# Optimization experiments

Hardware: AMD Instinct MI355X
Metric: run time of the kernel (lower is better)

## Reference

```python
import jax, jax.numpy as jnp
import numpy as np

B = 32; N = 512; SEQ_LEN = 8
L = 0.05; T_REF = 5.0; V_TH = 20.0; V_RES = 0.0
SQL = float(np.sqrt(L))
BN_EPS = 1e-5

# ---- Dawson-style lookup tables for the LIF moment activation (built once, float64) ----
_XG = np.linspace(-10.0, 4.0, 7001)
_DX = _XG[1] - _XG[0]

def _cumtrapz(y):
    return np.concatenate([[0.0], np.cumsum(0.5 * (y[1:] + y[:-1]) * _DX)])

_phi = np.exp(-_XG ** 2)
_I = np.exp(-100.0) / 20.0 + _cumtrapz(_phi)          # int_{-inf}^x e^{-t^2} dt (asymptotic tail at -10)
_g = np.exp(_XG ** 2) * _I                             # 1st Dawson-like function g(x)
_G = _cumtrapz(_g)                                     # int g dx (rel. to -10)
_h = np.exp(_XG ** 2) * _cumtrapz(_phi * _g ** 2)      # 2nd Dawson-like function h(x)
_H = _cumtrapz(_h)                                     # int h dx

XG = jnp.asarray(_XG, jnp.float32)
GT = jnp.asarray(_g, jnp.float32)
GI = jnp.asarray(_G, jnp.float32)
HI = jnp.asarray(_H, jnp.float32)

def _interp(x, tab):
    return jnp.interp(x, XG, tab)

def moment_activate(u, s, rho):
    # Mnn_Activate_Mean / Std / Corr: LIF moment activation
    s = jnp.maximum(s, 1e-6)
    ub = jnp.clip((V_TH * L - u) / (s * SQL), -10.0, 4.0)
    lb = jnp.clip((V_RES * L - u) / (s * SQL), -10.0, 4.0)
    dG = _interp(ub, GI) - _interp(lb, GI)
    ua = 1.0 / (T_REF + (2.0 / L) * dG)                               # mean firing rate
    dH = jnp.maximum(_interp(ub, HI) - _interp(lb, HI), 0.0)
    sa = jnp.sqrt((8.0 / L ** 2) * dH * ua ** 3)                      # firing std
    dg = _interp(ub, GT) - _interp(lb, GT)
    chi = ua ** 2 * (2.0 / L) * dg / (SQL * jnp.maximum(sa, 1e-9))    # linear response coeff
    eye = jnp.eye(rho.shape[-1], dtype=rho.dtype)
    rho_out = chi[:, :, None] * chi[:, None, :] * rho                 # [B,N,N]
    rho_out = rho_out * (1.0 - eye) + eye                             # unit diagonal
    return ua, sa, rho_out

def linear_corr(W, b, u, s, rho):
    # Mnn_Linear_Corr: mean via affine map, covariance via W C W^T
    u_out = u @ W.T + b
    Cin = rho * s[:, :, None] * s[:, None, :]                         # [B,N,N] covariance
    C = jnp.einsum('bik,lk->bil', jnp.einsum('ij,bjk->bik', W, Cin), W)
    var = jnp.clip(jnp.diagonal(C, axis1=1, axis2=2), 0.0, None)
    s_out = jnp.sqrt(var)
    denom = s_out[:, :, None] * s_out[:, None, :]
    rho_out = jnp.where(denom > 1e-12, C / jnp.maximum(denom, 1e-12), 0.0)
    return u_out, s_out, rho_out

def mexi_hat(n, k=0.3):
    dx = 2.0 * np.pi / n
    x = np.arange(0.0, 2.0 * np.pi, dx)[:n]
    y = np.exp(2.0 * (np.cos(x) - 1.0)) * np.cos(2.0 * x)
    j = np.arange(n)
    idx = (j[None, :] - j[:, None]) % n                               # w[i,:] = y.roll(i)
    return y[idx].astype(np.float32)

def setup_inputs() -> dict:
    ks = jax.random.split(jax.random.key(0), 10)
    u = jax.random.normal(ks[0], (B, N), jnp.float32)
    s = jax.random.uniform(ks[1], (B, N), jnp.float32, 0.1, 1.0)
    A = jax.random.normal(ks[2], (B, N, N), jnp.float32) / np.sqrt(N)
    sym = 0.5 * (A + jnp.swapaxes(A, 1, 2))
    eye = jnp.eye(N, dtype=jnp.float32)
    rho = jnp.clip(sym, -0.5, 0.5) * (1.0 - eye) + eye                # valid-ish corr matrix
    u_ext = jax.random.normal(ks[3], (B, N), jnp.float32)
    s_ext = jax.random.uniform(ks[4], (B, N), jnp.float32, 0.1, 1.0)
    W = 0.02 * jax.random.normal(ks[5], (N, N), jnp.float32) + 0.1 * jnp.asarray(mexi_hat(N))
    b = 0.02 * jax.random.normal(ks[6], (N,), jnp.float32)
    W_ext = 0.02 * jax.random.normal(ks[7], (N, N), jnp.float32)
    b_ext = 0.02 * jax.random.normal(ks[8], (N,), jnp.float32)
    w_mean = 2.5 * jnp.ones((N,), jnp.float32)
    b_mean = 2.5 * jnp.ones((N,), jnp.float32)
    w_mean_ext = 2.5 * jnp.ones((N,), jnp.float32)
    b_mean_ext = 2.5 * jnp.ones((N,), jnp.float32)
    return {'u': u, 's': s, 'rho': rho, 'u_ext': u_ext, 's_ext': s_ext,
            'W': W, 'b': b, 'W_ext': W_ext, 'b_ext': b_ext,
            'w_mean': w_mean, 'b_mean': b_mean,
            'w_mean_ext': w_mean_ext, 'b_mean_ext': b_mean_ext,
            'seq_len': SEQ_LEN}

def reference(u, s, rho, u_ext, s_ext, W, b, W_ext, b_ext,
              w_mean, b_mean, w_mean_ext, b_mean_ext, seq_len):
    # external pathway (Mnn_Linear_without_Corr + BN), computed once
    u_e = u_ext @ W_ext.T + b_ext
    s_e = jnp.sqrt((s_ext ** 2) @ (W_ext ** 2).T)
    mean_e = jnp.mean(u_e, axis=0); var_e = jnp.var(u_e, axis=0)
    f_e = w_mean_ext / jnp.sqrt(var_e + BN_EPS)
    s_e = s_e * jnp.abs(f_e)                                          # Mnn_Std_Bn1d (uses pre-BN stats)
    u_e = (u_e - mean_e) * f_e + b_mean_ext

    def step(carry, _):
        u, s, rho = carry
        u, s, rho = linear_corr(W, b, u, s, rho)
        mean = jnp.mean(u, axis=0); var = jnp.var(u, axis=0)
        f = w_mean / jnp.sqrt(var + BN_EPS)
        s = s * jnp.abs(f)
        u = (u - mean) * f + b_mean
        u = u + u_e
        s = jnp.sqrt(s * s + s_e * s_e)
        return moment_activate(u, s, rho), None

    (u, s, rho), _ = jax.lax.scan(step, (u, s, rho), None, length=seq_len)
    return u, s, rho
```

## Files before the change

### kernel.cpp

```cpp
#include <hip/hip_runtime.h>
#include <math.h>


#define BB 32
#define NN 512
#define SEQ 8
#define TG 7001
#define SVN (BB * NN)

typedef float f32x4 __attribute__((ext_vector_type(4)));
typedef short s16x8 __attribute__((ext_vector_type(8)));

__device__ __forceinline__ unsigned short bf16_rne(float v) {
    unsigned u = __float_as_uint(v);
    u += 0x7FFFu + ((u >> 16) & 1u);
    return (unsigned short)(u >> 16);
}
__device__ __forceinline__ float bf16_f(unsigned short h) {
    return __uint_as_float(((unsigned)h) << 16);
}
__device__ __forceinline__ void split2(float v, unsigned short& h, unsigned short& l) {
    unsigned short hh = bf16_rne(v);
    h = hh;
    l = bf16_rne(v - bf16_f(hh));
}

__device__ __forceinline__ size_t ts_idx(int r, int k) {
    return (size_t)(((r >> 4) * 16 + (k >> 5)) * 512 + ((k >> 3) & 3) * 128 + (r & 15) * 8 + (k & 7));
}

__device__ __forceinline__ float interp_tab(const float* __restrict__ tab, float x) {
    float t = (x + 10.0f) * 500.0f;
    t = fminf(fmaxf(t, 0.0f), 7000.0f);
    int i0 = (int)t;
    if (i0 > 6999) i0 = 6999;
    float fr = t - (float)i0;
    float a = tab[i0];
    float b = tab[i0 + 1];
    return fmaf(fr, b - a, a);
}

__global__ void k_exp(double* __restrict__ expP, double* __restrict__ expM) {
    int k = blockIdx.x * 256 + threadIdx.x;
    if (k >= TG) return;
    double x = -10.0 + (14.0 / 7000.0) * k;
    expP[k] = exp(x * x);
    expM[k] = exp(-x * x);
}

__device__ double blk_exscan(double part, double* wsum) {
    int t = threadIdx.x, lane = t & 63, wid = t >> 6;
    double run = part;
    #pragma unroll
    for (int off = 1; off < 64; off <<= 1) {
        double nv = __shfl_up(run, off);
        if (lane >= off) run += nv;
    }
    if (lane == 63) wsum[wid] = run;
    __syncthreads();
    if (t < 16) {
        double v = wsum[t];
        #pragma unroll
        for (int off = 1; off < 16; off <<= 1) {
            double nv = __shfl_up(v, off);
            if (lane >= off) v += nv;
        }
        wsum[t] = v;
    }
    __syncthreads();
    double base = (wid > 0) ? wsum[wid - 1] : 0.0;
    double ex = base + run - part;
    __syncthreads();
    return ex;
}

__global__ __launch_bounds__(1024)
void k_scan(const double* __restrict__ expP, const double* __restrict__ expM,
            float* __restrict__ GT, float* __restrict__ GI, float* __restrict__ HI) {
    __shared__ double ys[7008];
    __shared__ double wsum[16];
    const int t = threadIdx.x;
    const double dx = 14.0 / 7000.0;
    int k0 = t * 7, k1 = k0 + 7;
    if (k1 > TG) k1 = TG;
    if (k0 > TG) k0 = TG;
    int kls = (k0 < 1) ? 1 : k0;

    for (int k = k0; k < k1; ++k) ys[k] = expM[k];
    __syncthreads();

    double tmp[7];
    {
        double part = 0.0;
        for (int k = kls; k < k1; ++k) part += 0.5 * (ys[k - 1] + ys[k]) * dx;
        double run = blk_exscan(part, wsum) + exp(-100.0) / 20.0;
        int c = 0;
        for (int k = k0; k < k1; ++k) {
            if (k >= 1) run += 0.5 * (ys[k - 1] + ys[k]) * dx;
            tmp[c] = expP[k] * run;
            GT[k] = (float)tmp[c];
            ++c;
        }
        __syncthreads();
        c = 0;
        for (int k = k0; k < k1; ++k) ys[k] = tmp[c++];
        __syncthreads();
    }
    {
        double part = 0.0;
        for (int k = kls; k < k1; ++k) part += 0.5 * (ys[k - 1] + ys[k]) * dx;
        double run = blk_exscan(part, wsum);
        for (int k = k0; k < k1; ++k) {
            if (k >= 1) run += 0.5 * (ys[k - 1] + ys[k]) * dx;
            GI[k] = (float)run;
        }
        __syncthreads();
    }
    {
        double part = 0.0;
        for (int k = kls; k < k1; ++k) {
            double ya = expM[k - 1] * ys[k - 1] * ys[k - 1];
            double yb = expM[k] * ys[k] * ys[k];
            part += 0.5 * (ya + yb) * dx;
        }
        double run = blk_exscan(part, wsum);
        int c = 0;
        for (int k = k0; k < k1; ++k) {
            if (k >= 1) {
                double ya = expM[k - 1] * ys[k - 1] * ys[k - 1];
                double yb = expM[k] * ys[k] * ys[k];
                run += 0.5 * (ya + yb) * dx;
            }
            tmp[c++] = run;
        }
        __syncthreads();
        c = 0;
        for (int k = k0; k < k1; ++k) ys[k] = tmp[c++];
        __syncthreads();
    }
    {
        double part = 0.0;
        for (int k = kls; k < k1; ++k)
            part += 0.5 * (expP[k - 1] * ys[k - 1] + expP[k] * ys[k]) * dx;
        double run = blk_exscan(part, wsum);
        for (int k = k0; k < k1; ++k) {
            if (k >= 1) run += 0.5 * (expP[k - 1] * ys[k - 1] + expP[k] * ys[k]) * dx;
            HI[k] = (float)run;
        }
    }
}

__global__ void k_splitW(const float* __restrict__ W,
                         unsigned short* __restrict__ Wh, unsigned short* __restrict__ Wl) {
    int t = blockIdx.x * 256 + threadIdx.x;
    int r = t >> 6, c8 = t & 63;
    int k = c8 * 8;
    const float* src = W + (size_t)r * NN + k;
    s16x8 hv, lv;
    #pragma unroll
    for (int q = 0; q < 8; ++q) {
        unsigned short h, l;
        split2(src[q], h, l);
        hv[q] = (short)h; lv[q] = (short)l;
    }
    size_t o = ts_idx(r, k);
    *reinterpret_cast<s16x8*>(Wh + o) = hv;
    *reinterpret_cast<s16x8*>(Wl + o) = lv;
}

__global__ void k_splitQ(const float* __restrict__ rho, const float* __restrict__ s,
                         unsigned short* __restrict__ Qh, unsigned short* __restrict__ Ql) {
    int t = blockIdx.x * 256 + threadIdx.x;
    int b = t >> 15;
    int rem = t & 32767;
    int r = rem >> 6, c8 = rem & 63;
    int k = c8 * 8;
    const float* src = rho + ((size_t)b * NN + r) * NN + k;
    const float* sb = s + b * NN;
    float si = sb[r];
    s16x8 hv, lv;
    #pragma unroll
    for (int q = 0; q < 8; ++q) {
        float v = src[q] * si * sb[k + q];
        unsigned short h, l;
        split2(v, h, l);
        hv[q] = (short)h; lv[q] = (short)l;
    }
    size_t o = (size_t)b * NN * NN + ts_idx(r, k);
    *reinterpret_cast<s16x8*>(Qh + o) = hv;
    *reinterpret_cast<s16x8*>(Ql + o) = lv;
}

#define LOADF(AH, AL, BH, BL, OFF)                                             \
    {                                                                          \
        _Pragma("unroll") for (int t_ = 0; t_ < 4; ++t_)                       \
            AH[t_] = *reinterpret_cast<const s16x8*>(pAh + t_ * 8192 + (OFF)); \
        _Pragma("unroll") for (int t_ = 0; t_ < 4; ++t_)                       \
            BH[t_] = *reinterpret_cast<const s16x8*>(pBh + t_ * 8192 + (OFF)); \
        _Pragma("unroll") for (int t_ = 0; t_ < 4; ++t_)                       \
            AL[t_] = *reinterpret_cast<const s16x8*>(pAl + t_ * 8192 + (OFF)); \
        _Pragma("unroll") for (int t_ = 0; t_ < 4; ++t_)                       \
            BL[t_] = *reinterpret_cast<const s16x8*>(pBl + t_ * 8192 + (OFF)); \
    }

#define MFMAF(AH, AL, BH, BL)                                                  \
    {                                                                          \
        _Pragma("unroll") for (int m_ = 0; m_ < 4; ++m_)                       \
            _Pragma("unroll") for (int n_ = 0; n_ < 4; ++n_)                   \
                acc[m_][n_] = __builtin_amdgcn_mfma_f32_16x16x32_bf16(         \
                    AH[m_], BH[n_], acc[m_][n_], 0, 0, 0);                     \
        _Pragma("unroll") for (int m_ = 0; m_ < 4; ++m_)                       \
            _Pragma("unroll") for (int n_ = 0; n_ < 4; ++n_)                   \
                acc[m_][n_] = __builtin_amdgcn_mfma_f32_16x16x32_bf16(         \
                    AL[m_], BH[n_], acc[m_][n_], 0, 0, 0);                     \
        _Pragma("unroll") for (int m_ = 0; m_ < 4; ++m_)                       \
            _Pragma("unroll") for (int n_ = 0; n_ < 4; ++n_)                   \
                acc[m_][n_] = __builtin_amdgcn_mfma_f32_16x16x32_bf16(         \
                    AH[m_], BL[n_], acc[m_][n_], 0, 0, 0);                     \
    }

template <int PHASE>
__global__ __launch_bounds__(256)
__attribute__((amdgpu_waves_per_eu(2, 2)))
void gemm_ts(const unsigned short* __restrict__ Ah, const unsigned short* __restrict__ Al,
             long aStride,
             const unsigned short* __restrict__ Bh, const unsigned short* __restrict__ Bl,
             long bStride,
             unsigned short* __restrict__ Oh, unsigned short* __restrict__ Ol,
             float* __restrict__ Of,
             const float* __restrict__ Wf, float* __restrict__ sv,
             const float* __restrict__ u_prev, const float* __restrict__ bvec,
             float* __restrict__ u_linT,
             const float* __restrict__ bn_w, const float* __restrict__ bmv,
             const float* __restrict__ u_e, const float* __restrict__ s_e2,
             const float* __restrict__ GT, const float* __restrict__ GI,
             const float* __restrict__ HI,
             float* __restrict__ u_next, float* __restrict__ s_next) {
    __shared__ __align__(16) unsigned short stg[4 * 8192];
    __shared__ float slS[256], chS[256], snS[256];

    const int id = blockIdx.x;
    const int member = (id >> 3) & 3;
    const int g = (id & 7) | ((id >> 5) << 3);
    const int p = g & 3;
    const int b = g >> 2;
    const int xt = (PHASE == 0) ? p : member;
    const int yt = (PHASE == 0) ? member : p;
    const int i0 = yt * 128, j0 = xt * 128;
    const int tid = threadIdx.x;
    const int w = tid >> 6, lane = tid & 63;
    const int wqm = w >> 1, wqn = w & 1;

    const int laneo = lane * 8;
    const unsigned short* pAh = Ah + (size_t)b * aStride + (size_t)((i0 >> 4) + wqm * 4) * 8192 + laneo;
    const unsigned short* pAl = Al + (size_t)b * aStride + (size_t)((i0 >> 4) + wqm * 4) * 8192 + laneo;
    const unsigned short* pBh = Bh + (size_t)b * bStride + (size_t)((j0 >> 4) + wqn * 4) * 8192 + laneo;
    const unsigned short* pBl = Bl + (size_t)b * bStride + (size_t)((j0 >> 4) + wqn * 4) * 8192 + laneo;

    s16x8 fah0[4], fal0[4], fbh0[4], fbl0[4];
    s16x8 fah1[4], fal1[4], fbh1[4], fbl1[4];

    LOADF(fah0, fal0, fbh0, fbl0, 0);

    if (PHASE == 0) {
        const int tile16 = yt * 4 + xt;
        const int row = tile16 * 32 + (tid >> 3);
        const int seg = tid & 7;
        const float4* wr = (const float4*)(Wf + (size_t)row * NN + seg * 64);
        const float4* ur = (const float4*)(u_prev + b * NN + seg * 64);
        float a0 = 0.f, a1 = 0.f, a2 = 0.f, a3 = 0.f;
        #pragma unroll
        for (int kk = 0; kk < 16; ++kk) {
            float4 wv = wr[kk], uv = ur[kk];
            a0 = fmaf(wv.x, uv.x, a0);
            a1 = fmaf(wv.y, uv.y, a1);
            a2 = fmaf(wv.z, uv.z, a2);
            a3 = fmaf(wv.w, uv.w, a3);
        }
        float au = (a0 + a1) + (a2 + a3);
        au += __shfl_xor(au, 1);
        au += __shfl_xor(au, 2);
        au += __shfl_xor(au, 4);
        if (seg == 0) u_linT[row * BB + b] = au + bvec[row];
    } else {
        const int ii = (tid < 128) ? (i0 + tid) : (j0 + tid - 128);
        float vb[32];
        {
            const float4* ul = (const float4*)(u_linT + (size_t)ii * BB);
            #pragma unroll
            for (int q = 0; q < 8; ++q) {
                float4 t4 = ul[q];
                vb[q * 4 + 0] = t4.x; vb[q * 4 + 1] = t4.y;
                vb[q * 4 + 2] = t4.z; vb[q * 4 + 3] = t4.w;
            }
        }
        float m = 0.0f;
        #pragma unroll
        for (int bb = 0; bb < BB; ++bb) m += vb[bb];
        m *= (1.0f / BB);
        float v = 0.0f;
        #pragma unroll
        for (int bb = 0; bb < BB; ++bb) {
            float d = vb[bb] - m;
            v = fmaf(d, d, v);
        }
        v *= (1.0f / BB);
        float f = bn_w[ii] / sqrtf(v + 1e-5f);
        const int idx = b * NN + ii;
        float s2;
        {
            const float* svp = sv + idx;
            float p0 = svp[0 * SVN] + svp[1 * SVN];
            float p1 = svp[2 * SVN] + svp[3 * SVN];
            float p2 = svp[4 * SVN] + svp[5 * SVN];
            float p3 = svp[6 * SVN] + svp[7 * SVN];
            s2 = (p0 + p1) + (p2 + p3);
        }
        float s_l = sqrtf(fmaxf(s2, 0.0f));
        float un = fmaf(vb[b] - m, f, bmv[ii]) + u_e[idx];
        float sn = sqrtf(fmaf((s_l * s_l) * f, f, s_e2[idx]));
        const float SQL = 0.22360679774997896f;
        float ss = fmaxf(sn, 1e-6f);
        float inv = 1.0f / (ss * SQL);
        float ubx = fminf(fmaxf((1.0f - un) * inv, -10.0f), 4.0f);
        float lbx = fminf(fmaxf((0.0f - un) * inv, -10.0f), 4.0f);
        float dG = interp_tab(GI, ubx) - interp_tab(GI, lbx);
        float ua = 1.0f / fmaf(40.0f, dG, 5.0f);
        float dH = fmaxf(interp_tab(HI, ubx) - interp_tab(HI, lbx), 0.0f);
        float sa = sqrtf(3200.0f * dH * ua * ua * ua);
        float dg2 = interp_tab(GT, ubx) - interp_tab(GT, lbx);
        float ch = ua * ua * 40.0f * dg2 / (SQL * fmaxf(sa, 1e-9f));
        slS[tid] = s_l;
        chS[tid] = ch;
        snS[tid] = sa;
        if (i0 == j0 && tid < 128) {
            u_next[idx] = ua;
            s_next[idx] = sa;
        }
    }

    f32x4 acc[4][4];
    #pragma unroll
    for (int m2 = 0; m2 < 4; ++m2)
        #pragma unroll
        for (int n2 = 0; n2 < 4; ++n2) acc[m2][n2] = (f32x4){0.f, 0.f, 0.f, 0.f};

    #pragma unroll
    for (int kb = 0; kb < 14; kb += 2) {
        LOADF(fah1, fal1, fbh1, fbl1, (kb + 1) * 512);
        MFMAF(fah0, fal0, fbh0, fbl0);
        LOADF(fah0, fal0, fbh0, fbl0, (kb + 2) * 512);
        MFMAF(fah1, fal1, fbh1, fbl1);
    }
    LOADF(fah1, fal1, fbh1, fbl1, 15 * 512);
    MFMAF(fah0, fal0, fbh0, fbl0);
    MFMAF(fah1, fal1, fbh1, fbl1);

    if (PHASE != 0) __syncthreads();

    const size_t bofs = (size_t)b * NN * NN;
    const int rb0 = i0 + wqm * 64 + (lane >> 4) * 4;
    const int cb0 = j0 + wqn * 64 + (lane & 15);

    if (PHASE == 0) {
        float dp[16];
        #pragma unroll
        for (int m2 = 0; m2 < 4; ++m2)
            #pragma unroll
            for (int r = 0; r < 4; ++r) {
                int row = rb0 + m2 * 16 + r;
                const float* wrow = Wf + ((size_t)row << 9) + cb0;
                float s = 0.0f;
                #pragma unroll
                for (int n2 = 0; n2 < 4; ++n2) s = fmaf(acc[m2][n2][r], wrow[n2 * 16], s);
                dp[m2 * 4 + r] = s;
            }
        #pragma unroll
        for (int k = 0; k < 16; ++k) {
            #pragma unroll
            for (int off = 1; off < 16; off <<= 1) dp[k] += __shfl_xor(dp[k], off);
        }
        if ((lane & 15) == 0) {
            float* svslot = sv + (size_t)(xt * 2 + wqn) * SVN + b * NN;
            #pragma unroll
            for (int k = 0; k < 16; ++k) {
                int row = rb0 + (k >> 2) * 16 + (k & 3);
                svslot[row] = dp[k];
            }
        }
    }

    if (PHASE == 2) {
        float* fS = (float*)stg + w * 4096;
        const int lcf = ((lane >> 4) << 8) + (lane & 15);
        #pragma unroll
        for (int m2 = 0; m2 < 4; ++m2)
            #pragma unroll
            for (int r = 0; r < 4; ++r) {
                const int lr = m2 * 16 + (lane >> 4) * 4 + r;
                const float si = slS[wqm * 64 + lr], ci = chS[wqm * 64 + lr];
                const int row = i0 + wqm * 64 + lr;
                #pragma unroll
                for (int n2 = 0; n2 < 4; ++n2) {
                    const int lc = wqn * 64 + n2 * 16 + (lane & 15);
                    const float sj = slS[128 + lc], cj = chS[128 + lc];
                    const int col = j0 + lc;
                    float denom = si * sj;
                    float rv = (denom > 1e-12f) ? (acc[m2][n2][r] / fmaxf(denom, 1e-12f)) : 0.0f;
                    rv *= ci * cj;
                    if (row == col) rv = 1.0f;
                    fS[lcf + m2 * 1024 + r * 64 + n2 * 16] = rv;
                }
            }
        #pragma unroll
        for (int inst = 0; inst < 16; ++inst) {
            const int row = i0 + wqm * 64 + inst * 4 + (lane >> 4);
            const int col = j0 + wqn * 64 + (lane & 15) * 4;
            *reinterpret_cast<f32x4*>(Of + bofs + ((size_t)row << 9) + col) =
                *reinterpret_cast<const f32x4*>(fS + inst * 256 + (lane >> 4) * 64 + (lane & 15) * 4);
        }
    } else {
        unsigned short* hiS = stg + w * 8192;
        unsigned short* loS = hiS + 4096;
        const int laneconst = (((lane & 15) >> 3) << 7) + ((lane >> 4) << 5) + (lane & 7);
        #pragma unroll
        for (int m2 = 0; m2 < 4; ++m2)
            #pragma unroll
            for (int n2 = 0; n2 < 4; ++n2) {
                const int base = laneconst + m2 * 1024 + (n2 >> 1) * 512 + (n2 & 1) * 256;
                #pragma unroll
                for (int r = 0; r < 4; ++r) {
                    float v;
                    if (PHASE == 0) {
                        v = acc[m2][n2][r];
                    } else {
                        const int lr = wqm * 64 + m2 * 16 + (lane >> 4) * 4 + r;
                        const int lc = wqn * 64 + n2 * 16 + (lane & 15);
                        const float si = slS[lr], ci = chS[lr], qi = snS[lr];
                        const float sj = slS[128 + lc], cj = chS[128 + lc], qj = snS[128 + lc];
                        float denom = si * sj;
                        float rv = (denom > 1e-12f) ? (acc[m2][n2][r] / fmaxf(denom, 1e-12f)) : 0.0f;
                        rv *= ci * cj;
                        if (i0 + lr == j0 + lc) rv = 1.0f;
                        v = rv * qi * qj;
                    }
                    unsigned short h, l;
                    split2(v, h, l);
                    hiS[base + r * 8] = h;
                    loS[base + r * 8] = l;
                }
            }
        #pragma unroll
        for (int lb = 0; lb < 8; ++lb) {
            const int gb = ((i0 >> 4) + wqm * 4 + (lb >> 1)) * 16 + (j0 >> 5) + wqn * 2 + (lb & 1);
            *reinterpret_cast<s16x8*>(Oh + bofs + (size_t)gb * 512 + laneo) =
                *reinterpret_cast<const s16x8*>(hiS + lb * 512 + laneo);
            *reinterpret_cast<s16x8*>(Ol + bofs + (size_t)gb * 512 + laneo) =
                *reinterpret_cast<const s16x8*>(loS + lb * 512 + laneo);
        }
    }
}

__global__ void k_ext_dots(const float* __restrict__ Wx, const float* __restrict__ bx,
                           const float* __restrict__ ux, const float* __restrict__ sx,
                           float* __restrict__ u_e, float* __restrict__ s_e2) {
    int gw = (blockIdx.x << 2) + (threadIdx.x >> 6);
    int lane = threadIdx.x & 63;
    int b = gw >> 9, i = gw & 511;
    const float* wr = Wx + (size_t)i * NN;
    const float* ub = ux + b * NN;
    const float* sb = sx + b * NN;
    float au = 0.0f, as2 = 0.0f;
    for (int j = lane; j < NN; j += 64) {
        float w = wr[j];
        float s = sb[j];
        au = fmaf(w, ub[j], au);
        as2 = fmaf(w * w, s * s, as2);
    }
    #pragma unroll
    for (int off = 32; off; off >>= 1) {
        au += __shfl_down(au, off);
        as2 += __shfl_down(as2, off);
    }
    if (lane == 0) {
        u_e[b * NN + i] = au + bx[i];
        s_e2[b * NN + i] = as2;
    }
}

__global__ void k_ext_stats(float* __restrict__ u_e, float* __restrict__ s_e2,
                            const float* __restrict__ wmx, const float* __restrict__ bmx) {
    int i = blockIdx.x * blockDim.x + threadIdx.x;
    if (i >= NN) return;
    float m = 0.0f;
    for (int b = 0; b < BB; ++b) m += u_e[b * NN + i];
    m *= (1.0f / BB);
    float v = 0.0f;
    for (int b = 0; b < BB; ++b) {
        float d = u_e[b * NN + i] - m;
        v = fmaf(d, d, v);
    }
    v *= (1.0f / BB);
    float f = wmx[i] / sqrtf(v + 1e-5f);
    float bm = bmx[i];
    for (int b = 0; b < BB; ++b) {
        u_e[b * NN + i] = fmaf(u_e[b * NN + i] - m, f, bm);
        s_e2[b * NN + i] *= f * f;
    }
}

extern "C" void kernel_launch(void* const* d_in, const int* in_sizes, int n_in,
                              void* d_out, int out_size, void* d_ws, size_t ws_size,
                              hipStream_t stream) {
    (void)in_sizes; (void)n_in; (void)out_size; (void)ws_size;
    const float* u_in       = (const float*)d_in[0];
    const float* s_in       = (const float*)d_in[1];
    const float* rho_in     = (const float*)d_in[2];
    const float* u_ext      = (const float*)d_in[3];
    const float* s_ext      = (const float*)d_in[4];
    const float* W          = (const float*)d_in[5];
    const float* bvec       = (const float*)d_in[6];
    const float* W_ext      = (const float*)d_in[7];
    const float* b_ext      = (const float*)d_in[8];
    const float* w_mean     = (const float*)d_in[9];
    const float* b_mean     = (const float*)d_in[10];
    const float* w_mean_ext = (const float*)d_in[11];
    const float* b_mean_ext = (const float*)d_in[12];

    float* out_u   = (float*)d_out;
    float* out_s   = out_u + BB * NN;
    float* out_rho = out_s + BB * NN;
    unsigned short* Qh = (unsigned short*)out_rho;
    unsigned short* Ql = Qh + (size_t)BB * NN * NN;

    char* base = (char*)d_ws;
    size_t off = 0;
    auto alloc = [&](size_t bytes) -> char* {
        char* ptr = base + off;
        off += (bytes + 255) & ~(size_t)255;
        return ptr;
    };
    unsigned short* T1h = (unsigned short*)alloc((size_t)BB * NN * NN * 2);
    unsigned short* T1l = (unsigned short*)alloc((size_t)BB * NN * NN * 2);
    unsigned short* Wh  = (unsigned short*)alloc((size_t)NN * NN * 2);
    unsigned short* Wl  = (unsigned short*)alloc((size_t)NN * NN * 2);
    double* expP = (double*)alloc(TG * 8);
    double* expM = (double*)alloc(TG * 8);
    float* GTt   = (float*)alloc(TG * 4);
    float* GIt   = (float*)alloc(TG * 4);
    float* HIt   = (float*)alloc(TG * 4);
    float* u_e   = (float*)alloc(BB * NN * 4);
    float* s_e2  = (float*)alloc(BB * NN * 4);
    float* uA    = (float*)alloc(BB * NN * 4);
    float* uB2   = (float*)alloc(BB * NN * 4);
    float* sA    = (float*)alloc(BB * NN * 4);
    float* sB2   = (float*)alloc(BB * NN * 4);
    float* u_linT = (float*)alloc(BB * NN * 4);
    float* sv    = (float*)alloc((size_t)8 * BB * NN * 4);

    k_exp<<<28, 256, 0, stream>>>(expP, expM);
    k_scan<<<1, 1024, 0, stream>>>(expP, expM, GTt, GIt, HIt);
    k_splitW<<<128, 256, 0, stream>>>(W, Wh, Wl);
    k_splitQ<<<4096, 256, 0, stream>>>(rho_in, s_in, Qh, Ql);
    k_ext_dots<<<BB * NN / 4, 256, 0, stream>>>(W_ext, b_ext, u_ext, s_ext, u_e, s_e2);
    k_ext_stats<<<2, 256, 0, stream>>>(u_e, s_e2, w_mean_ext, b_mean_ext);

    const float* cu = u_in;

    for (int t = 0; t < SEQ; ++t) {
        gemm_ts<0><<<512, 256, 0, stream>>>(
            Wh, Wl, 0L, Qh, Ql, (long)NN * NN, T1h, T1l, nullptr,
            W, sv, cu, bvec, u_linT,
            nullptr, nullptr, nullptr, nullptr, nullptr, nullptr, nullptr,
            nullptr, nullptr);
        float* nu = (t == SEQ - 1) ? out_u : ((t & 1) ? uA : uB2);
        float* ns = (t == SEQ - 1) ? out_s : ((t & 1) ? sA : sB2);
        if (t < SEQ - 1) {
            gemm_ts<1><<<512, 256, 0, stream>>>(
                T1h, T1l, (long)NN * NN, Wh, Wl, 0L, Qh, Ql, nullptr,
                nullptr, sv, nullptr, nullptr, u_linT,
                w_mean, b_mean, u_e, s_e2, GTt, GIt, HIt, nu, ns);
        } else {
            gemm_ts<2><<<512, 256, 0, stream>>>(
                T1h, T1l, (long)NN * NN, Wh, Wl, 0L, nullptr, nullptr, out_rho,
                nullptr, sv, nullptr, nullptr, u_linT,
                w_mean, b_mean, u_e, s_e2, GTt, GIt, HIt, nu, ns);
        }
        cu = nu;
    }
}
```

Before: 781.2 us.

## Split GEMM tile across 8 waves with 64x32 per-wave subtiles

Each block now runs 512 threads (8 waves) instead of 256, each wave computing a 64x32 output subtile rather than 64x64. This halves the per-wave accumulator and fragment registers and drops the explicit double-buffered register prefetch in favour of a simple unroll-by-2 loop. The aim is more waves in flight to hide global-load latency. The row-sum partial buffer grows to 16 slots, and the epilogue and LDS staging layouts are reindexed to match. A-fragments are now loaded by twice as many waves, which raises redundant global/L2 traffic, and losing the explicit prefetch may expose latency.

Result: no change. 794.8 us (+1.7%).

```diff
diff --git a/kernel.cpp b/kernel.cpp
--- a/kernel.cpp
+++ b/kernel.cpp
@@ -195,33 +195,32 @@
     {                                                                          \
         _Pragma("unroll") for (int t_ = 0; t_ < 4; ++t_)                       \
             AH[t_] = *reinterpret_cast<const s16x8*>(pAh + t_ * 8192 + (OFF)); \
-        _Pragma("unroll") for (int t_ = 0; t_ < 4; ++t_)                       \
+        _Pragma("unroll") for (int t_ = 0; t_ < 2; ++t_)                       \
             BH[t_] = *reinterpret_cast<const s16x8*>(pBh + t_ * 8192 + (OFF)); \
         _Pragma("unroll") for (int t_ = 0; t_ < 4; ++t_)                       \
             AL[t_] = *reinterpret_cast<const s16x8*>(pAl + t_ * 8192 + (OFF)); \
-        _Pragma("unroll") for (int t_ = 0; t_ < 4; ++t_)                       \
+        _Pragma("unroll") for (int t_ = 0; t_ < 2; ++t_)                       \
             BL[t_] = *reinterpret_cast<const s16x8*>(pBl + t_ * 8192 + (OFF)); \
     }
 
 #define MFMAF(AH, AL, BH, BL)                                                  \
     {                                                                          \
         _Pragma("unroll") for (int m_ = 0; m_ < 4; ++m_)                       \
-            _Pragma("unroll") for (int n_ = 0; n_ < 4; ++n_)                   \
+            _Pragma("unroll") for (int n_ = 0; n_ < 2; ++n_)                   \
                 acc[m_][n_] = __builtin_amdgcn_mfma_f32_16x16x32_bf16(         \
                     AH[m_], BH[n_], acc[m_][n_], 0, 0, 0);                     \
         _Pragma("unroll") for (int m_ = 0; m_ < 4; ++m_)                       \
-            _Pragma("unroll") for (int n_ = 0; n_ < 4; ++n_)                   \
+            _Pragma("unroll") for (int n_ = 0; n_ < 2; ++n_)                   \
                 acc[m_][n_] = __builtin_amdgcn_mfma_f32_16x16x32_bf16(         \
                     AL[m_], BH[n_], acc[m_][n_], 0, 0, 0);                     \
         _Pragma("unroll") for (int m_ = 0; m_ < 4; ++m_)                       \
-            _Pragma("unroll") for (int n_ = 0; n_ < 4; ++n_)                   \
+            _Pragma("unroll") for (int n_ = 0; n_ < 2; ++n_)                   \
                 acc[m_][n_] = __builtin_amdgcn_mfma_f32_16x16x32_bf16(         \
                     AH[m_], BL[n_], acc[m_][n_], 0, 0, 0);                     \
     }
 
 template <int PHASE>
-__global__ __launch_bounds__(256)
-__attribute__((amdgpu_waves_per_eu(2, 2)))
+__global__ __launch_bounds__(512, 4)
 void gemm_ts(const unsigned short* __restrict__ Ah, const unsigned short* __restrict__ Al,
              long aStride,
              const unsigned short* __restrict__ Bh, const unsigned short* __restrict__ Bl,
@@ -236,7 +235,7 @@
              const float* __restrict__ GT, const float* __restrict__ GI,
              const float* __restrict__ HI,
              float* __restrict__ u_next, float* __restrict__ s_next) {
-    __shared__ __align__(16) unsigned short stg[4 * 8192];
+    __shared__ __align__(16) unsigned short stg[8 * 4096];
     __shared__ float slS[256], chS[256], snS[256];
 
     const int id = blockIdx.x;
@@ -249,28 +248,23 @@
     const int i0 = yt * 128, j0 = xt * 128;
     const int tid = threadIdx.x;
     const int w = tid >> 6, lane = tid & 63;
-    const int wqm = w >> 1, wqn = w & 1;
+    const int wqm = w >> 2, wqn = w & 3;
 
     const int laneo = lane * 8;
     const unsigned short* pAh = Ah + (size_t)b * aStride + (size_t)((i0 >> 4) + wqm * 4) * 8192 + laneo;
     const unsigned short* pAl = Al + (size_t)b * aStride + (size_t)((i0 >> 4) + wqm * 4) * 8192 + laneo;
-    const unsigned short* pBh = Bh + (size_t)b * bStride + (size_t)((j0 >> 4) + wqn * 4) * 8192 + laneo;
-    const unsigned short* pBl = Bl + (size_t)b * bStride + (size_t)((j0 >> 4) + wqn * 4) * 8192 + laneo;
-
-    s16x8 fah0[4], fal0[4], fbh0[4], fbl0[4];
-    s16x8 fah1[4], fal1[4], fbh1[4], fbl1[4];
-
-    LOADF(fah0, fal0, fbh0, fbl0, 0);
+    const unsigned short* pBh = Bh + (size_t)b * bStride + (size_t)((j0 >> 4) + wqn * 2) * 8192 + laneo;
+    const unsigned short* pBl = Bl + (size_t)b * bStride + (size_t)((j0 >> 4) + wqn * 2) * 8192 + laneo;
 
     if (PHASE == 0) {
         const int tile16 = yt * 4 + xt;
-        const int row = tile16 * 32 + (tid >> 3);
-        const int seg = tid & 7;
-        const float4* wr = (const float4*)(Wf + (size_t)row * NN + seg * 64);
-        const float4* ur = (const float4*)(u_prev + b * NN + seg * 64);
+        const int row = tile16 * 32 + (tid >> 4);
+        const int seg = tid & 15;
+        const float4* wr = (const float4*)(Wf + (size_t)row * NN + seg * 32);
+        const float4* ur = (const float4*)(u_prev + b * NN + seg * 32);
         float a0 = 0.f, a1 = 0.f, a2 = 0.f, a3 = 0.f;
         #pragma unroll
-        for (int kk = 0; kk < 16; ++kk) {
+        for (int kk = 0; kk < 8; ++kk) {
             float4 wv = wr[kk], uv = ur[kk];
             a0 = fmaf(wv.x, uv.x, a0);
             a1 = fmaf(wv.y, uv.y, a1);
@@ -281,8 +275,9 @@
         au += __shfl_xor(au, 1);
         au += __shfl_xor(au, 2);
         au += __shfl_xor(au, 4);
+        au += __shfl_xor(au, 8);
         if (seg == 0) u_linT[row * BB + b] = au + bvec[row];
-    } else {
+    } else if (tid < 256) {
         const int ii = (tid < 128) ? (i0 + tid) : (j0 + tid - 128);
         float vb[32];
         {
@@ -310,11 +305,11 @@
         float s2;
         {
             const float* svp = sv + idx;
-            float p0 = svp[0 * SVN] + svp[1 * SVN];
-            float p1 = svp[2 * SVN] + svp[3 * SVN];
-            float p2 = svp[4 * SVN] + svp[5 * SVN];
-            float p3 = svp[6 * SVN] + svp[7 * SVN];
-            s2 = (p0 + p1) + (p2 + p3);
+            float q0 = (svp[0 * SVN] + svp[1 * SVN]) + (svp[2 * SVN] + svp[3 * SVN]);
+            float q1 = (svp[4 * SVN] + svp[5 * SVN]) + (svp[6 * SVN] + svp[7 * SVN]);
+            float q2 = (svp[8 * SVN] + svp[9 * SVN]) + (svp[10 * SVN] + svp[11 * SVN]);
+            float q3 = (svp[12 * SVN] + svp[13 * SVN]) + (svp[14 * SVN] + svp[15 * SVN]);
+            s2 = (q0 + q1) + (q2 + q3);
         }
         float s_l = sqrtf(fmaxf(s2, 0.0f));
         float un = fmaf(vb[b] - m, f, bmv[ii]) + u_e[idx];
@@ -339,28 +334,24 @@
         }
     }
 
-    f32x4 acc[4][4];
+    f32x4 acc[4][2];
     #pragma unroll
     for (int m2 = 0; m2 < 4; ++m2)
         #pragma unroll
-        for (int n2 = 0; n2 < 4; ++n2) acc[m2][n2] = (f32x4){0.f, 0.f, 0.f, 0.f};
-
-    #pragma unroll
-    for (int kb = 0; kb < 14; kb += 2) {
-        LOADF(fah1, fal1, fbh1, fbl1, (kb + 1) * 512);
-        MFMAF(fah0, fal0, fbh0, fbl0);
-        LOADF(fah0, fal0, fbh0, fbl0, (kb + 2) * 512);
-        MFMAF(fah1, fal1, fbh1, fbl1);
-    }
-    LOADF(fah1, fal1, fbh1, fbl1, 15 * 512);
-    MFMAF(fah0, fal0, fbh0, fbl0);
-    MFMAF(fah1, fal1, fbh1, fbl1);
+        for (int n2 = 0; n2 < 2; ++n2) acc[m2][n2] = (f32x4){0.f, 0.f, 0.f, 0.f};
+
+    s16x8 fah[4], fal[4], fbh[2], fbl[2];
+    #pragma unroll 2
+    for (int kb = 0; kb < 16; ++kb) {
+        LOADF(fah, fal, fbh, fbl, kb * 512);
+        MFMAF(fah, fal, fbh, fbl);
+    }
 
     if (PHASE != 0) __syncthreads();
 
     const size_t bofs = (size_t)b * NN * NN;
     const int rb0 = i0 + wqm * 64 + (lane >> 4) * 4;
-    const int cb0 = j0 + wqn * 64 + (lane & 15);
+    const int cb0 = j0 + wqn * 32 + (lane & 15);
 
     if (PHASE == 0) {
         float dp[16];
@@ -372,7 +363,7 @@
                 const float* wrow = Wf + ((size_t)row << 9) + cb0;
                 float s = 0.0f;
                 #pragma unroll
-                for (int n2 = 0; n2 < 4; ++n2) s = fmaf(acc[m2][n2][r], wrow[n2 * 16], s);
+                for (int n2 = 0; n2 < 2; ++n2) s = fmaf(acc[m2][n2][r], wrow[n2 * 16], s);
                 dp[m2 * 4 + r] = s;
             }
         #pragma unroll
@@ -381,7 +372,7 @@
             for (int off = 1; off < 16; off <<= 1) dp[k] += __shfl_xor(dp[k], off);
         }
         if ((lane & 15) == 0) {
-            float* svslot = sv + (size_t)(xt * 2 + wqn) * SVN + b * NN;
+            float* svslot = sv + (size_t)(xt * 4 + wqn) * SVN + b * NN;
             #pragma unroll
             for (int k = 0; k < 16; ++k) {
                 int row = rb0 + (k >> 2) * 16 + (k & 3);
@@ -391,8 +382,7 @@
     }
 
     if (PHASE == 2) {
-        float* fS = (float*)stg + w * 4096;
-        const int lcf = ((lane >> 4) << 8) + (lane & 15);
+        float* fS = (float*)stg + w * 2048;
         #pragma unroll
         for (int m2 = 0; m2 < 4; ++m2)
             #pragma unroll
@@ -401,33 +391,33 @@
                 const float si = slS[wqm * 64 + lr], ci = chS[wqm * 64 + lr];
                 const int row = i0 + wqm * 64 + lr;
                 #pragma unroll
-                for (int n2 = 0; n2 < 4; ++n2) {
-                    const int lc = wqn * 64 + n2 * 16 + (lane & 15);
+                for (int n2 = 0; n2 < 2; ++n2) {
+                    const int lc = wqn * 32 + n2 * 16 + (lane & 15);
                     const float sj = slS[128 + lc], cj = chS[128 + lc];
                     const int col = j0 + lc;
                     float denom = si * sj;
                     float rv = (denom > 1e-12f) ? (acc[m2][n2][r] / fmaxf(denom, 1e-12f)) : 0.0f;
                     rv *= ci * cj;
                     if (row == col) rv = 1.0f;
-                    fS[lcf + m2 * 1024 + r * 64 + n2 * 16] = rv;
+                    fS[lr * 32 + n2 * 16 + (lane & 15)] = rv;
                 }
             }
         #pragma unroll
-        for (int inst = 0; inst < 16; ++inst) {
-            const int row = i0 + wqm * 64 + inst * 4 + (lane >> 4);
-            const int col = j0 + wqn * 64 + (lane & 15) * 4;
+        for (int inst = 0; inst < 8; ++inst) {
+            const int row = i0 + wqm * 64 + inst * 8 + (lane >> 3);
+            const int col = j0 + wqn * 32 + (lane & 7) * 4;
             *reinterpret_cast<f32x4*>(Of + bofs + ((size_t)row << 9) + col) =
-                *reinterpret_cast<const f32x4*>(fS + inst * 256 + (lane >> 4) * 64 + (lane & 15) * 4);
+                *reinterpret_cast<const f32x4*>(fS + inst * 256 + (lane >> 3) * 32 + (lane & 7) * 4);
         }
     } else {
-        unsigned short* hiS = stg + w * 8192;
-        unsigned short* loS = hiS + 4096;
+        unsigned short* hiS = stg + w * 4096;
+        unsigned short* loS = hiS + 2048;
         const int laneconst = (((lane & 15) >> 3) << 7) + ((lane >> 4) << 5) + (lane & 7);
         #pragma unroll
         for (int m2 = 0; m2 < 4; ++m2)
             #pragma unroll
-            for (int n2 = 0; n2 < 4; ++n2) {
-                const int base = laneconst + m2 * 1024 + (n2 >> 1) * 512 + (n2 & 1) * 256;
+            for (int n2 = 0; n2 < 2; ++n2) {
+                const int base = laneconst + m2 * 512 + n2 * 256;
                 #pragma unroll
                 for (int r = 0; r < 4; ++r) {
                     float v;
@@ -435,7 +425,7 @@
                         v = acc[m2][n2][r];
                     } else {
                         const int lr = wqm * 64 + m2 * 16 + (lane >> 4) * 4 + r;
-                        const int lc = wqn * 64 + n2 * 16 + (lane & 15);
+                        const int lc = wqn * 32 + n2 * 16 + (lane & 15);
                         const float si = slS[lr], ci = chS[lr], qi = snS[lr];
                         const float sj = slS[128 + lc], cj = chS[128 + lc], qj = snS[128 + lc];
                         float denom = si * sj;
@@ -451,8 +441,8 @@
                 }
             }
         #pragma unroll
-        for (int lb = 0; lb < 8; ++lb) {
-            const int gb = ((i0 >> 4) + wqm * 4 + (lb >> 1)) * 16 + (j0 >> 5) + wqn * 2 + (lb & 1);
+        for (int lb = 0; lb < 4; ++lb) {
+            const int gb = ((i0 >> 4) + wqm * 4 + lb) * 16 + (j0 >> 5) + wqn;
             *reinterpret_cast<s16x8*>(Oh + bofs + (size_t)gb * 512 + laneo) =
                 *reinterpret_cast<const s16x8*>(hiS + lb * 512 + laneo);
             *reinterpret_cast<s16x8*>(Ol + bofs + (size_t)gb * 512 + laneo) =
@@ -556,7 +546,7 @@
     float* sA    = (float*)alloc(BB * NN * 4);
     float* sB2   = (float*)alloc(BB * NN * 4);
     float* u_linT = (float*)alloc(BB * NN * 4);
-    float* sv    = (float*)alloc((size_t)8 * BB * NN * 4);
+    float* sv    = (float*)alloc((size_t)16 * BB * NN * 4);
 
     k_exp<<<28, 256, 0, stream>>>(expP, expM);
     k_scan<<<1, 1024, 0, stream>>>(expP, expM, GTt, GIt, HIt);
@@ -568,7 +558,7 @@
     const float* cu = u_in;
 
     for (int t = 0; t < SEQ; ++t) {
-        gemm_ts<0><<<512, 256, 0, stream>>>(
+        gemm_ts<0><<<512, 512, 0, stream>>>(
             Wh, Wl, 0L, Qh, Ql, (long)NN * NN, T1h, T1l, nullptr,
             W, sv, cu, bvec, u_linT,
             nullptr, nullptr, nullptr, nullptr, nullptr, nullptr, nullptr,
@@ -576,12 +566,12 @@
         float* nu = (t == SEQ - 1) ? out_u : ((t & 1) ? uA : uB2);
         float* ns = (t == SEQ - 1) ? out_s : ((t & 1) ? sA : sB2);
         if (t < SEQ - 1) {
-            gemm_ts<1><<<512, 256, 0, stream>>>(
+            gemm_ts<1><<<512, 512, 0, stream>>>(
                 T1h, T1l, (long)NN * NN, Wh, Wl, 0L, Qh, Ql, nullptr,
                 nullptr, sv, nullptr, nullptr, u_linT,
                 w_mean, b_mean, u_e, s_e2, GTt, GIt, HIt, nu, ns);
         } else {
-            gemm_ts<2><<<512, 256, 0, stream>>>(
+            gemm_ts<2><<<512, 512, 0, stream>>>(
                 T1h, T1l, (long)NN * NN, Wh, Wl, 0L, nullptr, nullptr, out_rho,
                 nullptr, sv, nullptr, nullptr, u_linT,
                 w_mean, b_mean, u_e, s_e2, GTt, GIt, HIt, nu, ns);
```

## Stage GEMM operands through LDS with global_load_lds double buffering

Applied to the files above, without the earlier changes.

Replaces per-wave direct global-to-register fragment loads with a cooperative double-buffered LDS staging scheme using global_load_lds, so each block loads every A/B hi/lo panel once and waves share it instead of each wave re-reading duplicated fragments. A barrier per k-step is added, and launch bounds change from a waves_per_eu attribute to a min-blocks hint. It trades duplicated global traffic for LDS reads and synchronisation overhead.

Measured after the change: 716.9 us. 8.2% less time.

```diff
diff --git a/kernel.cpp b/kernel.cpp
--- a/kernel.cpp
+++ b/kernel.cpp
@@ -39,6 +39,11 @@
     float b = tab[i0 + 1];
     return fmaf(fr, b - a, a);
 }
+
+#define GLOAD_LDS16(GP, LP)                                                        \
+    __builtin_amdgcn_global_load_lds(                                              \
+        (const __attribute__((address_space(1))) unsigned int*)(const void*)(GP),  \
+        (__attribute__((address_space(3))) unsigned int*)(void*)(LP), 16, 0, 0)
 
 __global__ void k_exp(double* __restrict__ expP, double* __restrict__ expM) {
     int k = blockIdx.x * 256 + threadIdx.x;
@@ -191,18 +196,6 @@
     *reinterpret_cast<s16x8*>(Ql + o) = lv;
 }
 
-#define LOADF(AH, AL, BH, BL, OFF)                                             \
-    {                                                                          \
-        _Pragma("unroll") for (int t_ = 0; t_ < 4; ++t_)                       \
-            AH[t_] = *reinterpret_cast<const s16x8*>(pAh + t_ * 8192 + (OFF)); \
-        _Pragma("unroll") for (int t_ = 0; t_ < 4; ++t_)                       \
-            BH[t_] = *reinterpret_cast<const s16x8*>(pBh + t_ * 8192 + (OFF)); \
-        _Pragma("unroll") for (int t_ = 0; t_ < 4; ++t_)                       \
-            AL[t_] = *reinterpret_cast<const s16x8*>(pAl + t_ * 8192 + (OFF)); \
-        _Pragma("unroll") for (int t_ = 0; t_ < 4; ++t_)                       \
-            BL[t_] = *reinterpret_cast<const s16x8*>(pBl + t_ * 8192 + (OFF)); \
-    }
-
 #define MFMAF(AH, AL, BH, BL)                                                  \
     {                                                                          \
         _Pragma("unroll") for (int m_ = 0; m_ < 4; ++m_)                       \
@@ -219,9 +212,15 @@
                     AH[m_], BL[n_], acc[m_][n_], 0, 0, 0);                     \
     }
 
+#define STAGE(BUFOFF, KB)                                                      \
+    {                                                                          \
+        _Pragma("unroll") for (int q_ = 0; q_ < 8; ++q_)                       \
+            GLOAD_LDS16(gp[q_] + (size_t)(KB) * 512,                           \
+                        stg + (BUFOFF) + (c0 + q_) * 512);                     \
+    }
+
 template <int PHASE>
-__global__ __launch_bounds__(256)
-__attribute__((amdgpu_waves_per_eu(2, 2)))
+__global__ __launch_bounds__(256, 2)
 void gemm_ts(const unsigned short* __restrict__ Ah, const unsigned short* __restrict__ Al,
              long aStride,
              const unsigned short* __restrict__ Bh, const unsigned short* __restrict__ Bl,
@@ -236,7 +235,7 @@
              const float* __restrict__ GT, const float* __restrict__ GI,
              const float* __restrict__ HI,
              float* __restrict__ u_next, float* __restrict__ s_next) {
-    __shared__ __align__(16) unsigned short stg[4 * 8192];
+    __shared__ __align__(16) unsigned short stg[2 * 16384];
     __shared__ float slS[256], chS[256], snS[256];
 
     const int id = blockIdx.x;
@@ -250,17 +249,22 @@
     const int tid = threadIdx.x;
     const int w = tid >> 6, lane = tid & 63;
     const int wqm = w >> 1, wqn = w & 1;
-
     const int laneo = lane * 8;
-    const unsigned short* pAh = Ah + (size_t)b * aStride + (size_t)((i0 >> 4) + wqm * 4) * 8192 + laneo;
-    const unsigned short* pAl = Al + (size_t)b * aStride + (size_t)((i0 >> 4) + wqm * 4) * 8192 + laneo;
-    const unsigned short* pBh = Bh + (size_t)b * bStride + (size_t)((j0 >> 4) + wqn * 4) * 8192 + laneo;
-    const unsigned short* pBl = Bl + (size_t)b * bStride + (size_t)((j0 >> 4) + wqn * 4) * 8192 + laneo;
-
-    s16x8 fah0[4], fal0[4], fbh0[4], fbl0[4];
-    s16x8 fah1[4], fal1[4], fbh1[4], fbl1[4];
-
-    LOADF(fah0, fal0, fbh0, fbl0, 0);
+
+    const int c0 = w * 8;
+    const unsigned short* gp[8];
+    #pragma unroll
+    for (int q = 0; q < 8; ++q) {
+        const int c = c0 + q;
+        const unsigned short* src;
+        if (c < 8)       src = Ah + (size_t)b * aStride + (size_t)((i0 >> 4) + c) * 8192;
+        else if (c < 16) src = Al + (size_t)b * aStride + (size_t)((i0 >> 4) + c - 8) * 8192;
+        else if (c < 24) src = Bh + (size_t)b * bStride + (size_t)((j0 >> 4) + c - 16) * 8192;
+        else             src = Bl + (size_t)b * bStride + (size_t)((j0 >> 4) + c - 24) * 8192;
+        gp[q] = src + laneo;
+    }
+
+    STAGE(0, 0);
 
     if (PHASE == 0) {
         const int tile16 = yt * 4 + xt;
@@ -345,18 +349,24 @@
         #pragma unroll
         for (int n2 = 0; n2 < 4; ++n2) acc[m2][n2] = (f32x4){0.f, 0.f, 0.f, 0.f};
 
-    #pragma unroll
-    for (int kb = 0; kb < 14; kb += 2) {
-        LOADF(fah1, fal1, fbh1, fbl1, (kb + 1) * 512);
-        MFMAF(fah0, fal0, fbh0, fbl0);
-        LOADF(fah0, fal0, fbh0, fbl0, (kb + 2) * 512);
-        MFMAF(fah1, fal1, fbh1, fbl1);
-    }
-    LOADF(fah1, fal1, fbh1, fbl1, 15 * 512);
-    MFMAF(fah0, fal0, fbh0, fbl0);
-    MFMAF(fah1, fal1, fbh1, fbl1);
-
-    if (PHASE != 0) __syncthreads();
+    __syncthreads();
+
+    #pragma unroll 2
+    for (int kb = 0; kb < 16; ++kb) {
+        const int cur = (kb & 1) * 16384;
+        if (kb < 15) STAGE(16384 - cur, kb + 1);
+        const unsigned short* lb = stg + cur;
+        s16x8 fah[4], fal[4], fbh[4], fbl[4];
+        #pragma unroll
+        for (int t = 0; t < 4; ++t) {
+            fah[t] = *reinterpret_cast<const s16x8*>(lb + (wqm * 4 + t) * 512 + laneo);
+            fal[t] = *reinterpret_cast<const s16x8*>(lb + (8 + wqm * 4 + t) * 512 + laneo);
+            fbh[t] = *reinterpret_cast<const s16x8*>(lb + (16 + wqn * 4 + t) * 512 + laneo);
+            fbl[t] = *reinterpret_cast<const s16x8*>(lb + (24 + wqn * 4 + t) * 512 + laneo);
+        }
+        MFMAF(fah, fal, fbh, fbl);
+        __syncthreads();
+    }
 
     const size_t bofs = (size_t)b * NN * NN;
     const int rb0 = i0 + wqm * 64 + (lane >> 4) * 4;
@@ -451,12 +461,12 @@
                 }
             }
         #pragma unroll
-        for (int lb = 0; lb < 8; ++lb) {
-            const int gb = ((i0 >> 4) + wqm * 4 + (lb >> 1)) * 16 + (j0 >> 5) + wqn * 2 + (lb & 1);
+        for (int lb_ = 0; lb_ < 8; ++lb_) {
+            const int gb = ((i0 >> 4) + wqm * 4 + (lb_ >> 1)) * 16 + (j0 >> 5) + wqn * 2 + (lb_ & 1);
             *reinterpret_cast<s16x8*>(Oh + bofs + (size_t)gb * 512 + laneo) =
-                *reinterpret_cast<const s16x8*>(hiS + lb * 512 + laneo);
+                *reinterpret_cast<const s16x8*>(hiS + lb_ * 512 + laneo);
             *reinterpret_cast<s16x8*>(Ol + bofs + (size_t)gb * 512 + laneo) =
-                *reinterpret_cast<const s16x8*>(loS + lb * 512 + laneo);
+                *reinterpret_cast<const s16x8*>(loS + lb_ * 512 + laneo);
         }
     }
 }
```
